# Optimization experiments

Hardware: AMD Instinct MI355X
Metric: run time of the kernel (lower is better)

## Reference

```python
import jax, jax.numpy as jnp
import numpy as np

B, I, O = 4096, 30000, 10000  # batch, input_features, output_features (I == 3*O)


def setup_inputs() -> dict:
    key = jax.random.key(0)
    k1, k2, k3 = jax.random.split(key, 3)
    stdv = (3.0 / I) ** 0.5
    x = jax.random.normal(k1, (B, I), dtype=jnp.float32)
    weight = jax.random.uniform(k2, (O, I), dtype=jnp.float32, minval=-stdv, maxval=stdv)
    bias = jax.random.normal(k3, (O,), dtype=jnp.float32) * 0.01
    return {"input": x, "weight": weight, "bias": bias}


def reference(input, weight, bias):
    # Original torch math: out = input @ (weight * mask).T + bias,
    # where mask[i//3, i] = 1. Only entries weight[i//3, i] survive, so we
    # gather that diagonal band and do a grouped (3-to-1) reduction instead
    # of a dense masked matmul.
    b, i = input.shape
    o = weight.shape[0]
    cols = jnp.arange(i)
    rows = cols // 3
    w_band = weight[rows, cols]                      # [I] active weights
    out = (input * w_band).reshape(b, o, 3).sum(-1)  # [B, O]
    return out + bias
```

## Files before the change

### kernel.cpp

```cpp
#include <hip/hip_runtime.h>

#define BATCH 4096
#define INF   30000
#define OUTF  10000

__global__ void gather_band_kernel(const float* __restrict__ weight,
                                   float* __restrict__ w_band) {
    int i = blockIdx.x * blockDim.x + threadIdx.x;
    if (i < INF) {
        int row = i / 3;
        w_band[i] = weight[(size_t)row * INF + i];
    }
}

#define GROUPS_PER_ROW (OUTF / 4)

__global__ __launch_bounds__(256)
void banded_matvec_kernel(const float* __restrict__ x,
                          const float* __restrict__ w_band,
                          const float* __restrict__ bias,
                          float* __restrict__ out) {
    int t = blockIdx.x * blockDim.x + threadIdx.x;
    int b = t / GROUPS_PER_ROW;
    int r = t - b * GROUPS_PER_ROW;

    const float4* xv = reinterpret_cast<const float4*>(x + (size_t)b * INF + (size_t)r * 12);
    const float4* wv = reinterpret_cast<const float4*>(w_band + (size_t)r * 12);

    float4 x0 = xv[0], x1 = xv[1], x2 = xv[2];
    float4 w0 = wv[0], w1 = wv[1], w2 = wv[2];
    float4 bb = *reinterpret_cast<const float4*>(bias + (size_t)r * 4);

    float4 o4;
    o4.x = fmaf(x0.z, w0.z, fmaf(x0.y, w0.y, x0.x * w0.x)) + bb.x;
    o4.y = fmaf(x1.y, w1.y, fmaf(x1.x, w1.x, x0.w * w0.w)) + bb.y;
    o4.z = fmaf(x2.x, w2.x, fmaf(x1.w, w1.w, x1.z * w1.z)) + bb.z;
    o4.w = fmaf(x2.w, w2.w, fmaf(x2.z, w2.z, x2.y * w2.y)) + bb.w;

    *reinterpret_cast<float4*>(out + (size_t)b * OUTF + (size_t)r * 4) = o4;
}

extern "C" void kernel_launch(void* const* d_in, const int* in_sizes, int n_in,
                              void* d_out, int out_size, void* d_ws, size_t ws_size,
                              hipStream_t stream) {
    const float* x      = (const float*)d_in[0];
    const float* weight = (const float*)d_in[1];
    const float* bias   = (const float*)d_in[2];
    float* out          = (float*)d_out;
    float* w_band       = (float*)d_ws;

    {
        int threads = 256;
        int blocks = (INF + threads - 1) / threads;
        gather_band_kernel<<<blocks, threads, 0, stream>>>(weight, w_band);
    }

    {
        int total = BATCH * GROUPS_PER_ROW;
        int threads = 256;
        int blocks = total / threads;
        banded_matvec_kernel<<<blocks, threads, 0, stream>>>(x, w_band, bias, out);
    }
}
```

Measured before the change: 131.3 us.

## Restructure banded matvec into coalesced flat float4 loads with LDS partial-sum exchange

The banded reduction is recast as a flat stream over x: each thread loads contiguous float4s (a stride of 1 float4 across threads instead of 3), computes phase-dependent partial sums of the 3-element groups that straddle float4 boundaries, and exchanges them through shared memory before each thread assembles one float4 of output. The goal is fully coalesced x reads, plus nontemporal loads so the large input stream does not pollute cache. In exchange it adds an LDS round trip, a barrier and modulo indexing for weight and bias.

```diff
diff --git a/kernel.cpp b/kernel.cpp
--- a/kernel.cpp
+++ b/kernel.cpp
@@ -3,6 +3,13 @@
 #define BATCH 4096
 #define INF   30000
 #define OUTF  10000
+
+#define F4_PER_BLOCK 768
+#define THREADS      256
+#define NBLOCKS      ((BATCH * (INF / 4)) / F4_PER_BLOCK)
+
+typedef float f32x4 __attribute__((ext_vector_type(4)));
+typedef float f32x2 __attribute__((ext_vector_type(2)));
 
 __global__ void gather_band_kernel(const float* __restrict__ weight,
                                    float* __restrict__ w_band) {
@@ -13,31 +20,55 @@
     }
 }
 
-#define GROUPS_PER_ROW (OUTF / 4)
+__global__ __launch_bounds__(THREADS)
+void banded_flat_kernel(const float* __restrict__ x,
+                        const float* __restrict__ w_band,
+                        const float* __restrict__ bias,
+                        float* __restrict__ out) {
+    __shared__ f32x2 P[F4_PER_BLOCK];
 
-__global__ __launch_bounds__(256)
-void banded_matvec_kernel(const float* __restrict__ x,
-                          const float* __restrict__ w_band,
-                          const float* __restrict__ bias,
-                          float* __restrict__ out) {
-    int t = blockIdx.x * blockDim.x + threadIdx.x;
-    int b = t / GROUPS_PER_ROW;
-    int r = t - b * GROUPS_PER_ROW;
+    const int i = threadIdx.x;
+    const unsigned base = (unsigned)blockIdx.x * F4_PER_BLOCK;
 
-    const float4* xv = reinterpret_cast<const float4*>(x + (size_t)b * INF + (size_t)r * 12);
-    const float4* wv = reinterpret_cast<const float4*>(w_band + (size_t)r * 12);
+    const f32x4* xv4 = reinterpret_cast<const f32x4*>(x);
+    const f32x4* wv4 = reinterpret_cast<const f32x4*>(w_band);
 
-    float4 x0 = xv[0], x1 = xv[1], x2 = xv[2];
-    float4 w0 = wv[0], w1 = wv[1], w2 = wv[2];
-    float4 bb = *reinterpret_cast<const float4*>(bias + (size_t)r * 4);
+    #pragma unroll
+    for (int c = 0; c < 3; ++c) {
+        const int k = i + c * THREADS;
+        const unsigned K = base + k;
 
-    float4 o4;
-    o4.x = fmaf(x0.z, w0.z, fmaf(x0.y, w0.y, x0.x * w0.x)) + bb.x;
-    o4.y = fmaf(x1.y, w1.y, fmaf(x1.x, w1.x, x0.w * w0.w)) + bb.y;
-    o4.z = fmaf(x2.x, w2.x, fmaf(x1.w, w1.w, x1.z * w1.z)) + bb.z;
-    o4.w = fmaf(x2.w, w2.w, fmaf(x2.z, w2.z, x2.y * w2.y)) + bb.w;
+        f32x4 xv = __builtin_nontemporal_load(xv4 + (size_t)K);
+        f32x4 wv = wv4[K % 7500u];
 
-    *reinterpret_cast<float4*>(out + (size_t)b * OUTF + (size_t)r * 4) = o4;
+        const float d0 = xv.x * wv.x;
+        const float d1 = xv.y * wv.y;
+        const float d2 = xv.z * wv.z;
+        const float d3 = xv.w * wv.w;
+
+        const int ph = (i + c) % 3;
+        f32x2 pr;
+        pr.x = d0 + (ph <= 1 ? d1 : 0.f) + (ph == 0 ? d2 : 0.f);
+        pr.y = d3 + (ph >= 1 ? d2 : 0.f) + (ph == 2 ? d1 : 0.f);
+        P[k] = pr;
+    }
+
+    __syncthreads();
+
+    const f32x2 a = P[3 * i];
+    const f32x2 b = P[3 * i + 1];
+    const f32x2 c2 = P[3 * i + 2];
+
+    const unsigned G = (unsigned)blockIdx.x * THREADS + i;
+    const f32x4 bb = reinterpret_cast<const f32x4*>(bias)[G % 2500u];
+
+    f32x4 o;
+    o.x = a.x + bb.x;
+    o.y = a.y + b.x + bb.y;
+    o.z = b.y + c2.x + bb.z;
+    o.w = c2.y + bb.w;
+
+    reinterpret_cast<f32x4*>(out)[(size_t)G] = o;
 }
 
 extern "C" void kernel_launch(void* const* d_in, const int* in_sizes, int n_in,
@@ -55,10 +86,5 @@
         gather_band_kernel<<<blocks, threads, 0, stream>>>(weight, w_band);
     }
 
-    {
-        int total = BATCH * GROUPS_PER_ROW;
-        int threads = 256;
-        int blocks = total / threads;
-        banded_matvec_kernel<<<blocks, threads, 0, stream>>>(x, w_band, bias, out);
-    }
+    banded_flat_kernel<<<NBLOCKS, THREADS, 0, stream>>>(x, w_band, bias, out);
 }
```

New measurement: 122.7 us. 1.07x faster.
